# Performance work log

Hardware: AMD Instinct MI355X
Metric: run time of the kernel (lower is better)

Reference implementation:

```python
import jax, jax.numpy as jnp
import numpy as np

B, C, N = 8, 3, 4096
NSAMPLE = 10
MLP = (64, 64)
# checkerboard re-gather pattern from the original module
INDS = np.array([0, 1, 2, 3, 2, 3, 4, 5, 4, 5, 6, 7, 6, 7, 8, 9])


def setup_inputs() -> dict:
    key = jax.random.key(0)
    k1, k2, k3 = jax.random.split(key, 3)
    pos = jax.random.normal(k1, (B, C, N), jnp.float32)
    w1 = jax.random.normal(k2, (MLP[0], 4 * C, 2, 2), jnp.float32) * 0.1  # Conv2d(12, mlp0, k=2)
    b1 = jnp.zeros((MLP[0],), jnp.float32)
    w2 = jax.random.normal(k3, (MLP[1], MLP[0]), jnp.float32) * 0.1       # Conv2d(mlp0, mlp1, k=1)
    b2 = jnp.zeros((MLP[1],), jnp.float32)
    return {"pos": pos, "w1": w1, "b1": b1, "w2": w2, "b2": b2}


def _squeeze_2x2_alt(x):
    # x: [B, N, c, 4, 4] -> [B, N, 4c, 2, 2] with channel order [a, d, b, c]
    a = x[..., 0::2, 0::2]  # (0,0) of each 2x2 block
    d = x[..., 1::2, 1::2]  # (1,1)
    b = x[..., 0::2, 1::2]  # (0,1)
    c = x[..., 1::2, 0::2]  # (1,0)
    return jnp.concatenate([a, d, b, c], axis=-3)


def reference(pos, w1, b1, w2, b2):
    Bn, Cn, Nn = pos.shape
    pos_t = pos.transpose(0, 2, 1)  # [B, N, C]
    # pairwise squared distances [B, N, N]
    sq = jnp.sum(pos_t * pos_t, axis=-1)
    d2 = sq[:, :, None] - 2.0 * jnp.einsum('bnc,bmc->bnm', pos_t, pos_t) + sq[:, None, :]
    _, idx = jax.lax.top_k(-d2, NSAMPLE)  # [B, N, K] nearest neighbors (self first)
    # grouping_operation: grouped[b,c,n,k] = pos[b,c,idx[b,n,k]]
    grouped = jax.vmap(lambda p, i: p[:, i])(pos, idx)  # [B, C, N, K]
    pg = grouped[..., INDS]                              # [B, C, N, 16]
    pg = pg.transpose(0, 2, 1, 3).reshape(Bn, Nn, Cn, 4, 4)  # [B, N, 3, 4, 4]
    sqz = _squeeze_2x2_alt(pg)                           # [B, N, 12, 2, 2]
    # Conv2d(12->mlp0, k=2, stride=1) over 2x2 spatial == full contraction
    h = jnp.einsum('bnchw,ochw->bno', sqz, w1) + b1      # [B, N, mlp0]
    out = jnp.einsum('bno,po->bnp', h, w2) + b2          # [B, N, mlp1]
    return out.transpose(0, 2, 1)                        # [B, mlp1, N]
```

## Files before the change

### kernel.cpp

```cpp
#include <hip/hip_runtime.h>
#include <math.h>

#define NPTS 4096
#define NSMP 10

typedef _Float16 half4 __attribute__((ext_vector_type(4)));
typedef _Float16 half8 __attribute__((ext_vector_type(8)));
typedef float f32x4 __attribute__((ext_vector_type(4)));

__global__ __launch_bounds__(256) void prep_kernel(
    const float* __restrict__ w1, const float* __restrict__ b1,
    const float* __restrict__ w2, const float* __restrict__ b2,
    float* __restrict__ wn, float* __restrict__ bb) {
  __shared__ float w1l[64 * 48];
  __shared__ float w2t[64 * 64];
  __shared__ float b1l[64];
  __shared__ float part[4][30][64];
  __shared__ float bpart[4][64];
  const int t = threadIdx.x, p = t & 63, grp = t >> 6, o0 = grp * 16;
  for (int idx = t; idx < 64 * 48; idx += 256) w1l[idx] = w1[idx];
  for (int idx = t; idx < 64 * 64; idx += 256) w2t[(idx & 63) * 64 + (idx >> 6)] = w2[idx];
  if (t < 64) b1l[t] = b1[t];
  __syncthreads();

  const int sg[16] = {0,2,4,6, 3,5,7,9, 1,3,5,7, 2,4,6,8};
  float w2r[16];
  #pragma unroll
  for (int oo = 0; oo < 16; ++oo) w2r[oo] = w2t[(o0 + oo) * 64 + p];
  float wloc[30];
  #pragma unroll
  for (int i = 0; i < 30; ++i) wloc[i] = 0.0f;
  #pragma unroll
  for (int g = 0; g < 4; ++g)
    #pragma unroll
    for (int i = 0; i < 2; ++i)
      #pragma unroll
      for (int j = 0; j < 2; ++j) {
        const int s = sg[g * 4 + i * 2 + j];
        #pragma unroll
        for (int c = 0; c < 3; ++c) {
          const int k = (c + 3 * g) * 4 + i * 2 + j;
          float wk = 0.0f;
          #pragma unroll
          for (int oo = 0; oo < 16; ++oo)
            wk = fmaf(w2r[oo], w1l[(o0 + oo) * 48 + k], wk);
          wloc[s * 3 + c] += wk;
        }
      }
  #pragma unroll
  for (int i = 0; i < 30; ++i) part[grp][i][p] = wloc[i];
  float sb = 0.0f;
  #pragma unroll
  for (int oo = 0; oo < 16; ++oo) sb = fmaf(w2r[oo], b1l[o0 + oo], sb);
  bpart[grp][p] = sb;
  __syncthreads();
  const float* p0 = &part[0][0][0];
  for (int idx = t; idx < 30 * 64; idx += 256)
    wn[idx] = p0[idx] + p0[1920 + idx] + p0[3840 + idx] + p0[5760 + idx];
  if (t < 64) bb[t] = b2[t] + bpart[0][t] + bpart[1][t] + bpart[2][t] + bpart[3][t];
}

__global__ __launch_bounds__(1024, 5) void topk_kernel(const float* __restrict__ pos,
                                                       const float* __restrict__ wng,
                                                       const float* __restrict__ bbg,
                                                       float* __restrict__ out) {
  __shared__ half4 pts4[NPTS];
  __shared__ float X[16 * 260];
  __shared__ half4 a4s[64];
  __shared__ float wl[30 * 64];
  __shared__ float bl[64];
  __shared__ float taub[64];
  __shared__ float sqqs[64];
  __shared__ int   cnt[64];
  __shared__ int   nbrT[64][NSMP];

  const int b = blockIdx.y, tid = threadIdx.x, lane = tid & 63, wv = tid >> 6;
  const float* pb = pos + (size_t)b * 3 * NPTS;
  const int nb = blockIdx.x * 64;

  for (int i = tid; i < NPTS; i += 1024) {
    float x = pb[i], y = pb[i + NPTS], z = pb[i + 2 * NPTS];
    float sq = fmaf(z, z, fmaf(y, y, x * x));
    half4 v = {(_Float16)x, (_Float16)y, (_Float16)z, (_Float16)sq};
    pts4[i] = v;
  }
  if (tid < 64) {
    float qx = pb[nb + tid], qy = pb[nb + tid + NPTS], qz = pb[nb + tid + 2 * NPTS];
    half4 va = {(_Float16)(-2.0f * (float)(_Float16)qx),
                (_Float16)(-2.0f * (float)(_Float16)qy),
                (_Float16)(-2.0f * (float)(_Float16)qz),
                (_Float16)1.0f};
    a4s[tid] = va;
    sqqs[tid] = fmaf(qz, qz, fmaf(qy, qy, qx * qx));
    cnt[tid] = 0;
    bl[tid] = bbg[tid];
  }
  for (int i = tid; i < 30 * 64; i += 1024) wl[i] = wng[i];
  __syncthreads();

  const int qt = wv >> 2, ws = wv & 3, g = lane >> 4, col = lane & 15;
  const int base = ws * 1024;
  const int rowb = qt * 16 + g * 4;
  half8 af;
  #pragma unroll
  for (int j = 0; j < 8; ++j) af[j] = (_Float16)0.0f;
  if (g == 0) {
    half4 aq = a4s[qt * 16 + col];
    af[0] = aq[0]; af[1] = aq[1]; af[2] = aq[2]; af[3] = aq[3];
  }
  f32x4 zz;
  #pragma unroll
  for (int j = 0; j < 4; ++j) zz[j] = 0.0f;

  float mreg[4];
  #pragma unroll
  for (int j = 0; j < 4; ++j) mreg[j] = INFINITY;
  #pragma unroll 2
  for (int t = 0; t < 64; ++t) {
    half4 bp = pts4[base + t * 16 + col];
    half8 bf;
    bf[0] = bp[0]; bf[1] = bp[1]; bf[2] = bp[2]; bf[3] = bp[3];
    bf[4] = bp[0]; bf[5] = bp[1]; bf[6] = bp[2]; bf[7] = bp[3];
    f32x4 acc = __builtin_amdgcn_mfma_f32_16x16x32_f16(af, bf, zz, 0, 0, 0);
    #pragma unroll
    for (int j = 0; j < 4; ++j) mreg[j] = fminf(mreg[j], acc[j]);
  }
  #pragma unroll
  for (int j = 0; j < 4; ++j)
    X[(rowb + j) * 65 + ws * 16 + col] = mreg[j];
  __syncthreads();

  unsigned um[4];
  #pragma unroll
  for (int r = 0; r < 4; ++r) {
    float dm = X[(4 * wv + r) * 65 + lane];
    unsigned ub = __float_as_uint(dm);
    um[r] = (ub & 0x80000000u) ? ~ub : (ub | 0x80000000u);
  }
  unsigned pfx0 = 0u, pfx1 = 0u, pfx2 = 0u, pfx3 = 0u;
  #pragma unroll 1
  for (int bno = 31; bno >= 8; --bno) {
    const unsigned bit = 1u << bno, ones = bit - 1u;
    if (__popcll(__ballot(um[0] <= (pfx0 | ones))) < NSMP) pfx0 |= bit;
    if (__popcll(__ballot(um[1] <= (pfx1 | ones))) < NSMP) pfx1 |= bit;
    if (__popcll(__ballot(um[2] <= (pfx2 | ones))) < NSMP) pfx2 |= bit;
    if (__popcll(__ballot(um[3] <= (pfx3 | ones))) < NSMP) pfx3 |= bit;
  }
  float tx[4];
  #pragma unroll
  for (int r = 0; r < 4; ++r) {
    unsigned T = ((r == 0) ? pfx0 : (r == 1) ? pfx1 : (r == 2) ? pfx2 : pfx3) | 0xFFu;
    unsigned tb = (T & 0x80000000u) ? (T ^ 0x80000000u) : ~T;
    float tf = __uint_as_float(tb);
    float sqr = sqqs[4 * wv + r];
    float d10sq = tf + sqr;
    if (d10sq < 0.0f) d10sq = 0.0f;
    float aq = sqrtf(sqr);
    float L = aq + sqrtf(d10sq) + 0.05f;
    float slack = 2e-3f + 0.00146484375f * (4.0f * aq * L + L * L);
    tx[r] = __fadd_rn(tf, slack);
  }
  if (lane == 0) {
    taub[4 * wv + 0] = tx[0]; taub[4 * wv + 1] = tx[1];
    taub[4 * wv + 2] = tx[2]; taub[4 * wv + 3] = tx[3];
  }
  __syncthreads();

  float tau4[4];
  #pragma unroll
  for (int j = 0; j < 4; ++j) tau4[j] = taub[rowb + j];
  int* bufi = (int*)X;
  #pragma unroll 2
  for (int t = 0; t < 64; ++t) {
    const int m0 = base + t * 16 + col;
    half4 bp = pts4[m0];
    half8 bf;
    bf[0] = bp[0]; bf[1] = bp[1]; bf[2] = bp[2]; bf[3] = bp[3];
    bf[4] = bp[0]; bf[5] = bp[1]; bf[6] = bp[2]; bf[7] = bp[3];
    f32x4 acc = __builtin_amdgcn_mfma_f32_16x16x32_f16(af, bf, zz, 0, 0, 0);
    #pragma unroll
    for (int j = 0; j < 4; ++j) {
      if (acc[j] <= tau4[j]) {
        const int row = rowb + j;
        int ps = atomicAdd(&cnt[row], 1);
        if (ps < 64) bufi[row * 64 + ps] = m0;
      }
    }
  }
  __syncthreads();

  #pragma unroll 1
  for (int r = 0; r < 4; ++r) {
    const int row = 4 * wv + r;
    int cr = __builtin_amdgcn_readfirstlane(cnt[row]);
    if (cr > 64) cr = 64;
    const int nq = nb + row;
    int sv = 0x7FFFFFFF;
    double dv = (double)INFINITY;
    if (lane < cr) {
      float qxf = pb[nq], qyf = pb[nq + NPTS], qzf = pb[nq + 2 * NPTS];
      sv = bufi[row * 64 + lane];
      float px = pb[sv], py = pb[sv + NPTS], pz = pb[sv + 2 * NPTS];
      double dqx = (double)qxf, dqy = (double)qyf, dqz = (double)qzf;
      double dpx = (double)px, dpy = (double)py, dpz = (double)pz;
      double dot = dqx * dpx + dqy * dpy + dqz * dpz;
      double sqn = dqx * dqx + dqy * dqy + dqz * dqz;
      double sqm = dpx * dpx + dpy * dpy + dpz * dpz;
      dv = (sqn - 2.0 * dot) + sqm;
    }
    int rank = 0;
    #pragma unroll 1
    for (int j = 0; j < cr; ++j) {
      int jlo = __builtin_amdgcn_readlane(__double2loint(dv), j);
      int jhi = __builtin_amdgcn_readlane(__double2hiint(dv), j);
      int ji  = __builtin_amdgcn_readlane(sv, j);
      double jd = __hiloint2double(jhi, jlo);
      if (jd < dv || (jd == dv && ji < sv)) ++rank;
    }
    if (lane < cr && rank < NSMP)
      nbrT[row][rank] = sv;
  }
  __syncthreads();

  float* transF = &X[wv * 260];
  #pragma unroll 1
  for (int r = 0; r < 4; ++r) {
    float a = bl[lane];
    #pragma unroll
    for (int s = 0; s < NSMP; ++s) {
      const int id = nbrT[4 * wv + r][s];
      float px = pb[id], py = pb[id + NPTS], pz = pb[id + 2 * NPTS];
      a = fmaf(wl[(s * 3 + 0) * 64 + lane], px, a);
      a = fmaf(wl[(s * 3 + 1) * 64 + lane], py, a);
      a = fmaf(wl[(s * 3 + 2) * 64 + lane], pz, a);
    }
    transF[r * 65 + lane] = a;
  }
  __syncthreads();

  {
    int p = tid >> 4, t16 = tid & 15;
    float4 v;
    v.x = X[t16 * 260 + 0 * 65 + p];
    v.y = X[t16 * 260 + 1 * 65 + p];
    v.z = X[t16 * 260 + 2 * 65 + p];
    v.w = X[t16 * 260 + 3 * 65 + p];
    *(float4*)(out + ((size_t)b * 64 + p) * NPTS + nb + 4 * t16) = v;
  }
}

extern "C" void kernel_launch(void* const* d_in, const int* in_sizes, int n_in,
                              void* d_out, int out_size, void* d_ws, size_t ws_size,
                              hipStream_t stream) {
  (void)in_sizes; (void)n_in; (void)out_size; (void)ws_size;
  const float* pos = (const float*)d_in[0];
  const float* w1  = (const float*)d_in[1];
  const float* b1  = (const float*)d_in[2];
  const float* w2  = (const float*)d_in[3];
  const float* b2  = (const float*)d_in[4];
  float* out = (float*)d_out;

  float* wn = (float*)d_ws;
  float* bb = (float*)((char*)d_ws + 30 * 64 * 4);

  prep_kernel<<<dim3(1), dim3(256), 0, stream>>>(w1, b1, w2, b2, wn, bb);
  topk_kernel<<<dim3(64, 8), dim3(1024), 0, stream>>>(pos, wn, bb, out);
}
```

Baseline: 146.6 us.

## Fuse weight-folding prep into topk kernel using spare waves

```diff
diff --git a/kernel.cpp b/kernel.cpp
--- a/kernel.cpp
+++ b/kernel.cpp
@@ -8,64 +8,14 @@
 typedef _Float16 half8 __attribute__((ext_vector_type(8)));
 typedef float f32x4 __attribute__((ext_vector_type(4)));
 
-__global__ __launch_bounds__(256) void prep_kernel(
-    const float* __restrict__ w1, const float* __restrict__ b1,
-    const float* __restrict__ w2, const float* __restrict__ b2,
-    float* __restrict__ wn, float* __restrict__ bb) {
-  __shared__ float w1l[64 * 48];
-  __shared__ float w2t[64 * 64];
-  __shared__ float b1l[64];
-  __shared__ float part[4][30][64];
-  __shared__ float bpart[4][64];
-  const int t = threadIdx.x, p = t & 63, grp = t >> 6, o0 = grp * 16;
-  for (int idx = t; idx < 64 * 48; idx += 256) w1l[idx] = w1[idx];
-  for (int idx = t; idx < 64 * 64; idx += 256) w2t[(idx & 63) * 64 + (idx >> 6)] = w2[idx];
-  if (t < 64) b1l[t] = b1[t];
-  __syncthreads();
-
-  const int sg[16] = {0,2,4,6, 3,5,7,9, 1,3,5,7, 2,4,6,8};
-  float w2r[16];
-  #pragma unroll
-  for (int oo = 0; oo < 16; ++oo) w2r[oo] = w2t[(o0 + oo) * 64 + p];
-  float wloc[30];
-  #pragma unroll
-  for (int i = 0; i < 30; ++i) wloc[i] = 0.0f;
-  #pragma unroll
-  for (int g = 0; g < 4; ++g)
-    #pragma unroll
-    for (int i = 0; i < 2; ++i)
-      #pragma unroll
-      for (int j = 0; j < 2; ++j) {
-        const int s = sg[g * 4 + i * 2 + j];
-        #pragma unroll
-        for (int c = 0; c < 3; ++c) {
-          const int k = (c + 3 * g) * 4 + i * 2 + j;
-          float wk = 0.0f;
-          #pragma unroll
-          for (int oo = 0; oo < 16; ++oo)
-            wk = fmaf(w2r[oo], w1l[(o0 + oo) * 48 + k], wk);
-          wloc[s * 3 + c] += wk;
-        }
-      }
-  #pragma unroll
-  for (int i = 0; i < 30; ++i) part[grp][i][p] = wloc[i];
-  float sb = 0.0f;
-  #pragma unroll
-  for (int oo = 0; oo < 16; ++oo) sb = fmaf(w2r[oo], b1l[o0 + oo], sb);
-  bpart[grp][p] = sb;
-  __syncthreads();
-  const float* p0 = &part[0][0][0];
-  for (int idx = t; idx < 30 * 64; idx += 256)
-    wn[idx] = p0[idx] + p0[1920 + idx] + p0[3840 + idx] + p0[5760 + idx];
-  if (t < 64) bb[t] = b2[t] + bpart[0][t] + bpart[1][t] + bpart[2][t] + bpart[3][t];
-}
-
 __global__ __launch_bounds__(1024, 5) void topk_kernel(const float* __restrict__ pos,
-                                                       const float* __restrict__ wng,
-                                                       const float* __restrict__ bbg,
+                                                       const float* __restrict__ w1,
+                                                       const float* __restrict__ b1,
+                                                       const float* __restrict__ w2,
+                                                       const float* __restrict__ b2,
                                                        float* __restrict__ out) {
   __shared__ half4 pts4[NPTS];
-  __shared__ float X[16 * 260];
+  __shared__ __align__(16) float U[7936];
   __shared__ half4 a4s[64];
   __shared__ float wl[30 * 64];
   __shared__ float bl[64];
@@ -77,14 +27,58 @@
   const int b = blockIdx.y, tid = threadIdx.x, lane = tid & 63, wv = tid >> 6;
   const float* pb = pos + (size_t)b * 3 * NPTS;
   const int nb = blockIdx.x * 64;
-
-  for (int i = tid; i < NPTS; i += 1024) {
-    float x = pb[i], y = pb[i + NPTS], z = pb[i + 2 * NPTS];
-    float sq = fmaf(z, z, fmaf(y, y, x * x));
-    half4 v = {(_Float16)x, (_Float16)y, (_Float16)z, (_Float16)sq};
-    pts4[i] = v;
-  }
+  float* part = U;
+  float* bpart = U + 7680;
+  float* X = U;
+
+  if (wv < 12) {
+    for (int i = tid; i < NPTS; i += 768) {
+      float x = pb[i], y = pb[i + NPTS], z = pb[i + 2 * NPTS];
+      float sq = fmaf(z, z, fmaf(y, y, x * x));
+      half4 v = {(_Float16)x, (_Float16)y, (_Float16)z, (_Float16)sq};
+      pts4[i] = v;
+    }
+  } else {
+    const int t = tid - 768;
+    const int p = t & 63, grp = t >> 6, o0 = grp * 16;
+    const int sg[16] = {0,2,4,6, 3,5,7,9, 1,3,5,7, 2,4,6,8};
+    float w2r[16];
+    const float* w2p = w2 + p * 64 + o0;
+    #pragma unroll
+    for (int oo = 0; oo < 16; ++oo) w2r[oo] = w2p[oo];
+    #pragma unroll 1
+    for (int c = 0; c < 3; ++c) {
+      float wloc10[10];
+      #pragma unroll
+      for (int s = 0; s < 10; ++s) wloc10[s] = 0.0f;
+      #pragma unroll
+      for (int g = 0; g < 4; ++g)
+        #pragma unroll
+        for (int ii = 0; ii < 2; ++ii)
+          #pragma unroll
+          for (int jj = 0; jj < 2; ++jj) {
+            const int s = sg[g * 4 + ii * 2 + jj];
+            const int k = (c + 3 * g) * 4 + ii * 2 + jj;
+            float wk = 0.0f;
+            #pragma unroll
+            for (int oo = 0; oo < 16; ++oo)
+              wk = fmaf(w2r[oo], w1[(o0 + oo) * 48 + k], wk);
+            wloc10[s] += wk;
+          }
+      #pragma unroll
+      for (int s = 0; s < 10; ++s) part[grp * 1920 + (s * 3 + c) * 64 + p] = wloc10[s];
+    }
+    float sb = 0.0f;
+    #pragma unroll
+    for (int oo = 0; oo < 16; ++oo) sb = fmaf(w2r[oo], b1[o0 + oo], sb);
+    bpart[grp * 64 + p] = sb;
+  }
+  __syncthreads();
+
+  for (int idx = tid; idx < 30 * 64; idx += 1024)
+    wl[idx] = part[idx] + part[1920 + idx] + part[3840 + idx] + part[5760 + idx];
   if (tid < 64) {
+    bl[tid] = b2[tid] + bpart[tid] + bpart[64 + tid] + bpart[128 + tid] + bpart[192 + tid];
     float qx = pb[nb + tid], qy = pb[nb + tid + NPTS], qz = pb[nb + tid + 2 * NPTS];
     half4 va = {(_Float16)(-2.0f * (float)(_Float16)qx),
                 (_Float16)(-2.0f * (float)(_Float16)qy),
@@ -93,9 +87,7 @@
     a4s[tid] = va;
     sqqs[tid] = fmaf(qz, qz, fmaf(qy, qy, qx * qx));
     cnt[tid] = 0;
-    bl[tid] = bbg[tid];
-  }
-  for (int i = tid; i < 30 * 64; i += 1024) wl[i] = wng[i];
+  }
   __syncthreads();
 
   const int qt = wv >> 2, ws = wv & 3, g = lane >> 4, col = lane & 15;
@@ -252,7 +244,7 @@
 extern "C" void kernel_launch(void* const* d_in, const int* in_sizes, int n_in,
                               void* d_out, int out_size, void* d_ws, size_t ws_size,
                               hipStream_t stream) {
-  (void)in_sizes; (void)n_in; (void)out_size; (void)ws_size;
+  (void)in_sizes; (void)n_in; (void)out_size; (void)d_ws; (void)ws_size;
   const float* pos = (const float*)d_in[0];
   const float* w1  = (const float*)d_in[1];
   const float* b1  = (const float*)d_in[2];
@@ -260,9 +252,5 @@
   const float* b2  = (const float*)d_in[4];
   float* out = (float*)d_out;
 
-  float* wn = (float*)d_ws;
-  float* bb = (float*)((char*)d_ws + 30 * 64 * 4);
-
-  prep_kernel<<<dim3(1), dim3(256), 0, stream>>>(w1, b1, w2, b2, wn, bb);
-  topk_kernel<<<dim3(64, 8), dim3(1024), 0, stream>>>(pos, wn, bb, out);
+  topk_kernel<<<dim3(64, 8), dim3(1024), 0, stream>>>(pos, w1, b1, w2, b2, out);
 }
```

New measurement: 164.8 us. 1.12x slower.
